# Kernel optimization log

Hardware: AMD Instinct MI355X
Metric: run time of the kernel (lower is better)

The kernel has to match this reference:

```python
import jax, jax.numpy as jnp
import numpy as np

K = 3
KK = K * K
PAD = 1          # kernel_size // 2
MAX_SHIFT = 8.0  # bias_range > 0
DEG = 2          # degrees = (2, 2), paon_type 'a'


def setup_inputs() -> dict:
    key = jax.random.key(0)
    ks = jax.random.split(key, 6)
    B, C, O, H, W = 4, 64, 64, 160, 160
    x = jax.random.normal(ks[0], (B, C, H, W), jnp.float32)
    # offset conv is 1x1: weight [2*K*K, C], bias [2*K*K]
    off_w = jax.random.normal(ks[1], (2 * KK, C), jnp.float32) * 0.1
    off_b = jax.random.normal(ks[2], (2 * KK,), jnp.float32) * 0.1
    scale = 1.0 / np.sqrt(C * KK).astype(np.float32)
    w_m = jax.random.normal(ks[3], (DEG * O, C, K, K), jnp.float32) * scale
    w_n = jax.random.normal(ks[4], (DEG * O, C, K, K), jnp.float32) * scale
    w0 = jax.random.normal(ks[5], (O,), jnp.float32) * 0.1
    return {"x": x, "off_w": off_w, "off_b": off_b, "w_m": w_m, "w_n": w_n, "w0": w0}


def _bilinear_sample(x, py, px):
    """x: [B,C,H,W]; py,px: [B,KK,H,W] -> [B,C,KK,H,W]; zero outside bounds."""
    B, C, H, W = x.shape
    xf = x.reshape(B, C, H * W)
    y0 = jnp.floor(py)
    x0 = jnp.floor(px)
    wy = py - y0
    wx = px - x0
    y0i = y0.astype(jnp.int32)
    x0i = x0.astype(jnp.int32)
    out = jnp.zeros((B, C) + py.shape[1:], x.dtype)
    corners = ((0, 0, (1 - wy) * (1 - wx)), (0, 1, (1 - wy) * wx),
               (1, 0, wy * (1 - wx)), (1, 1, wy * wx))
    for dy, dx, wgt in corners:
        yy = y0i + dy
        xx = x0i + dx
        valid = (yy >= 0) & (yy < H) & (xx >= 0) & (xx < W)
        idx = jnp.clip(yy, 0, H - 1) * W + jnp.clip(xx, 0, W - 1)
        g = jax.vmap(lambda f, i: f[:, i])(xf, idx.reshape(B, -1))  # [B,C,KK*H*W]
        out = out + g.reshape(B, C, *py.shape[1:]) * (wgt * valid)[:, None]
    return out


def _after_poly_a(y, ch, o, take_abs):
    # channel reorder + groupwise sum, per PaLaBase.after_poly_a
    order = np.array([(k * ch) % (ch * o) + k // o for k in range(ch * o)])
    y = y[:, order].reshape(y.shape[0], ch, o, *y.shape[2:])
    return jnp.abs(y).sum(2) if take_abs else y.sum(2)


def reference(x, off_w, off_b, w_m, w_n, w0):
    B, C, H, W = x.shape
    O = w0.shape[0]
    # --- DeformOffset: 1x1 conv -> clamp to image -> tanh soft-limit ---
    off_r = jnp.einsum('bchw,oc->bohw', x, off_w) + off_b[None, :, None, None]
    gy = jnp.arange(H, dtype=x.dtype)[None, None, :, None]
    gx = jnp.arange(W, dtype=x.dtype)[None, None, None, :]
    oy = jnp.clip(off_r[:, 0::2], -gy, H - gy)  # [B,KK,H,W] (dy per kernel pos)
    ox = jnp.clip(off_r[:, 1::2], -gx, W - gx)  # [B,KK,H,W] (dx per kernel pos)
    soft = lambda o: jnp.where(jnp.abs(o) >= MAX_SHIFT,
                               MAX_SHIFT * jnp.tanh(o / MAX_SHIFT), o)
    oy, ox = soft(oy), soft(ox)
    # --- deformable sampling grid (stride=1, dilation=1, zero padding) ---
    kidx = jnp.arange(KK)
    kh = (kidx // K).astype(x.dtype)[None, :, None, None]
    kw = (kidx % K).astype(x.dtype)[None, :, None, None]
    base_y = (jnp.arange(H, dtype=x.dtype) - PAD)[None, None, :, None]
    base_x = (jnp.arange(W, dtype=x.dtype) - PAD)[None, None, None, :]
    py = base_y + kh + oy
    px = base_x + kw + ox
    samp = _bilinear_sample(x, py, px)  # [B,C,KK,H,W]
    # --- Pade numerator / denominator convs on the sampled tensor ---
    pm_raw = jnp.einsum('bckhw,ock->bohw', samp, w_m.reshape(DEG * O, C, KK))
    qn_raw = jnp.einsum('bckhw,ock->bohw', samp, w_n.reshape(DEG * O, C, KK))
    pm = _after_poly_a(pm_raw, O, DEG, take_abs=False)
    qn = _after_poly_a(qn_raw, O, DEG, take_abs=True)
    # prepare_for_div_a: (pm + w0, 1 + qn)
    return (pm + w0[None, :, None, None]) / (1.0 + qn)
```

## Files before the change

### kernel.cpp

```cpp
#include <hip/hip_runtime.h>
#include <hip/hip_bf16.h>
#include <hip/hip_fp16.h>

#define Hh 160
#define Ww 160
#define Cc 64
#define HWc 25600
#define Bb 4
#define AST 76

typedef __attribute__((ext_vector_type(8))) _Float16 half8;
typedef __attribute__((ext_vector_type(4))) float f32x4;

__device__ __forceinline__ unsigned int f2h2u(float a, float b) {
  __half2 h = __floats2half2_rn(a, b);
  return *(unsigned int*)&h;
}

__global__ __launch_bounds__(256) void k_prep(
    const float* __restrict__ x, const float* __restrict__ wm,
    const float* __restrict__ wn, const float* __restrict__ ow,
    unsigned short* __restrict__ xT, unsigned short* __restrict__ bf) {
  if (blockIdx.x < 400) {
    __shared__ unsigned short s[64][260];
    int wg = blockIdx.x;
    int b = wg / 100;
    int pix0 = (wg % 100) * 256;
    int l = threadIdx.x & 63, wv = threadIdx.x >> 6;
    const float* xb = x + (size_t)b * Cc * HWc + pix0;
#pragma unroll
    for (int i = 0; i < 16; i++) {
      int c = i * 4 + wv;
      float4 v = *(const float4*)&xb[(size_t)c * HWc + l * 4];
      *(uint2*)&s[c][l * 4] = make_uint2(f2h2u(v.x, v.y), f2h2u(v.z, v.w));
    }
    __syncthreads();
    int p = threadIdx.x;
    unsigned int w[32];
#pragma unroll
    for (int j = 0; j < 32; j++) {
      unsigned int a = s[2 * j][p];
      unsigned int bb = s[2 * j + 1][p];
      w[j] = (a & 0xffffu) | (bb << 16);
    }
    unsigned short* dst = xT + ((size_t)(b * HWc + pix0 + p)) * 64;
#pragma unroll
    for (int j = 0; j < 8; j++)
      ((uint4*)dst)[j] = make_uint4(w[4 * j], w[4 * j + 1], w[4 * j + 2], w[4 * j + 3]);
  } else {
    int i = (blockIdx.x - 400) * 256 + threadIdx.x;
    if (i < 9 * 2 * 12 * 64 * 8) {
      int j2 = i & 7;
      int lane = (i >> 3) & 63;
      int ntck = i >> 9;
      int nt = ntck % 12;
      int ck = ntck / 12;
      int kk = ck >> 1;
      int chunk = ck & 1;
      int n = nt * 16 + (lane & 15);
      int c = chunk * 32 + (lane >> 4) * 8 + j2;
      float v;
      if (n < 64)
        v = wm[(n * 64 + c) * 9 + kk] + wm[((n + 64) * 64 + c) * 9 + kk];
      else
        v = wn[((n - 64) * 64 + c) * 9 + kk];
      __half hv = __float2half_rn(v);
      bf[i] = *(unsigned short*)&hv;
    } else if (i < 9 * 2 * 12 * 64 * 8 + 2 * 2 * 64 * 8) {
      int j = i - 9 * 2 * 12 * 64 * 8;
      int j2 = j & 7;
      int lane = (j >> 3) & 63;
      int rest = j >> 9;
      int ntile = rest & 1;
      int chunk = rest >> 1;
      int n = ntile * 16 + (lane & 15);
      int c = chunk * 32 + (lane >> 4) * 8 + j2;
      if (n < 18) {
        __half hv = __float2half_rn(ow[n * 64 + c]);
        bf[i] = *(unsigned short*)&hv;
      } else {
        bf[i] = 0;
      }
    }
  }
}

__device__ __forceinline__ void gather_issue(const char* __restrict__ gbase,
                                             uint4 D, int chB, uint4& c00,
                                             uint4& c01, uint4& c10,
                                             uint4& c11) {
  int bb = (int)D.x + chB;
  int dxB = (int)(D.y & 0xffffu);
  int dyB = (int)(D.y >> 16);
  c00 = *(const uint4*)(gbase + bb);
  c01 = *(const uint4*)(gbase + bb + dxB);
  c10 = *(const uint4*)(gbase + bb + dyB);
  c11 = *(const uint4*)(gbase + bb + dxB + dyB);
}

__device__ __forceinline__ void combine_write(unsigned short* Arow, uint2 Wzw,
                                              const uint4& c00, const uint4& c01,
                                              const uint4& c10,
                                              const uint4& c11) {
  __half2 wz = *(const __half2*)&Wzw.x;
  __half2 ww = *(const __half2*)&Wzw.y;
  __half2 W00 = __half2half2(__low2half(wz));
  __half2 W01 = __half2half2(__high2half(wz));
  __half2 W10 = __half2half2(__low2half(ww));
  __half2 W11 = __half2half2(__high2half(ww));
  const unsigned int* a = (const unsigned int*)&c00;
  const unsigned int* b = (const unsigned int*)&c01;
  const unsigned int* c = (const unsigned int*)&c10;
  const unsigned int* d = (const unsigned int*)&c11;
  unsigned int o[4];
#pragma unroll
  for (int j = 0; j < 4; j++) {
    __half2 ha = *(const __half2*)&a[j];
    __half2 hb = *(const __half2*)&b[j];
    __half2 hc = *(const __half2*)&c[j];
    __half2 hd = *(const __half2*)&d[j];
    __half2 r = __hfma2(ha, W00,
                        __hfma2(hb, W01, __hfma2(hc, W10, __hmul2(hd, W11))));
    o[j] = *(unsigned int*)&r;
  }
  *(uint4*)Arow = make_uint4(o[0], o[1], o[2], o[3]);
}

__global__ __launch_bounds__(256, 4) void k_main(
    const unsigned short* __restrict__ xT, const float* __restrict__ w0,
    const float* __restrict__ off_b, const unsigned short* __restrict__ bfrag,
    const unsigned short* __restrict__ obfrag, float* __restrict__ out) {
  __shared__ unsigned short A[3][64 * AST];
  __shared__ uint4 gdesc[576];
  float2* spy = (float2*)&A[0][0];
  const uint2* gdw = (const uint2*)gdesc;
  const int tid = threadIdx.x;
  const int wg = blockIdx.x;
  const int band = wg & 7;
  const int local = wg >> 3;
  const int b = local / 50;
  const int pix0 = band * 3200 + (local % 50) * 64;
  const int wv = tid >> 6;
  const int l = tid & 63;
  const int lm = l & 15;
  const int quad = l >> 4;
  const int ch8 = l & 7;
  const int pr = l >> 3;
  const int chB = ch8 * 16;
  const int pl0 = wv * 16 + pr;
  const int pl1 = wv * 16 + 8 + pr;

  const unsigned short* xTb = xT + (size_t)b * HWc * 64;
  const char* gbase = (const char*)xTb;

  f32x4 acc[3][4];
  const f32x4 zero = {0.f, 0.f, 0.f, 0.f};
#pragma unroll
  for (int j = 0; j < 3; j++)
#pragma unroll
    for (int pt = 0; pt < 4; pt++) acc[j][pt] = zero;

  {
    f32x4 aO0 = zero, aO1 = zero;
    const unsigned short* xrow = xTb + (size_t)(pix0 + wv * 16 + lm) * 64;
#pragma unroll
    for (int chunk = 0; chunk < 2; chunk++) {
      half8 sb = *(const half8*)(xrow + chunk * 32 + quad * 8);
      half8 wf0 = *(const half8*)&obfrag[((chunk * 2 + 0) * 64 + l) * 8];
      half8 wf1 = *(const half8*)&obfrag[((chunk * 2 + 1) * 64 + l) * 8];
      aO0 = __builtin_amdgcn_mfma_f32_16x16x32_f16(wf0, sb, aO0, 0, 0, 0);
      aO1 = __builtin_amdgcn_mfma_f32_16x16x32_f16(wf1, sb, aO1, 0, 0, 0);
    }
    int pix = pix0 + wv * 16 + lm;
    int h = pix / Ww, w = pix % Ww;
    float fh = (float)h, fw = (float)w;
#pragma unroll
    for (int rr = 0; rr < 2; rr++) {
      int n = quad * 4 + 2 * rr;
      int kk = n >> 1;
      float oy = aO0[2 * rr] + off_b[n];
      float ox = aO0[2 * rr + 1] + off_b[n + 1];
      oy = fminf(fmaxf(oy, -fh), 160.0f - fh);
      ox = fminf(fmaxf(ox, -fw), 160.0f - fw);
      if (fabsf(oy) >= 8.0f) oy = 8.0f * tanhf(oy * 0.125f);
      if (fabsf(ox) >= 8.0f) ox = 8.0f * tanhf(ox * 0.125f);
      spy[kk * 64 + wv * 16 + lm] =
          make_float2(fh - 1.0f + (float)(kk / 3) + oy,
                      fw - 1.0f + (float)(kk % 3) + ox);
    }
    if (quad == 0) {
      float oy = aO1[0] + off_b[16];
      float ox = aO1[1] + off_b[17];
      oy = fminf(fmaxf(oy, -fh), 160.0f - fh);
      ox = fminf(fmaxf(ox, -fw), 160.0f - fw);
      if (fabsf(oy) >= 8.0f) oy = 8.0f * tanhf(oy * 0.125f);
      if (fabsf(ox) >= 8.0f) ox = 8.0f * tanhf(ox * 0.125f);
      spy[8 * 64 + wv * 16 + lm] =
          make_float2(fh + 1.0f + oy, fw + 1.0f + ox);
    }
  }
  __syncthreads();

  for (int e = tid; e < 576; e += 256) {
    float2 P = spy[e];
    float py = P.x, pxv = P.y;
    float y0f = floorf(py), x0f = floorf(pxv);
    float wy = py - y0f, wx = pxv - x0f;
    int y0 = (int)y0f, x0 = (int)x0f;
    float vy0 = (y0 >= 0 && y0 < Hh) ? 1.f : 0.f;
    float vy1 = (y0 >= -1 && y0 < Hh - 1) ? 1.f : 0.f;
    float vx0 = (x0 >= 0 && x0 < Ww) ? 1.f : 0.f;
    float vx1 = (x0 >= -1 && x0 < Ww - 1) ? 1.f : 0.f;
    int r0 = min(max(y0, 0), Hh - 1);
    int r1 = min(max(y0 + 1, 0), Hh - 1);
    int c0 = min(max(x0, 0), Ww - 1);
    int c1 = min(max(x0 + 1, 0), Ww - 1);
    float w00 = (1.f - wy) * (1.f - wx) * vy0 * vx0;
    float w01 = (1.f - wy) * wx * vy0 * vx1;
    float w10 = wy * (1.f - wx) * vy1 * vx0;
    float w11 = wy * wx * vy1 * vx1;
    uint4 D;
    D.x = (unsigned int)((r0 * Ww + c0) * 128);
    D.y = (unsigned int)((c1 - c0) * 128) |
          ((unsigned int)((r1 - r0) * Ww * 128) << 16);
    D.z = f2h2u(w00, w01);
    D.w = f2h2u(w10, w11);
    gdesc[e] = D;
  }
  __syncthreads();

  uint4 gA[8], gB[8];
  {
    uint4 D0 = gdesc[pl0], D1 = gdesc[pl1];
    gather_issue(gbase, D0, chB, gA[0], gA[1], gA[2], gA[3]);
    gather_issue(gbase, D1, chB, gA[4], gA[5], gA[6], gA[7]);
    uint4 E0 = gdesc[64 + pl0], E1 = gdesc[64 + pl1];
    gather_issue(gbase, E0, chB, gB[0], gB[1], gB[2], gB[3]);
    gather_issue(gbase, E1, chB, gB[4], gB[5], gB[6], gB[7]);
    combine_write(&A[0][pl0 * AST + ch8 * 8], make_uint2(D0.z, D0.w), gA[0],
                  gA[1], gA[2], gA[3]);
    combine_write(&A[0][pl1 * AST + ch8 * 8], make_uint2(D1.z, D1.w), gA[4],
                  gA[5], gA[6], gA[7]);
  }
  asm volatile("s_waitcnt lgkmcnt(0)" ::: "memory");
  __builtin_amdgcn_s_barrier();

#pragma unroll
  for (int kk = 0; kk < 9; kk++) {
    if (kk < 7) {
      uint4 D0 = gdesc[(kk + 2) * 64 + pl0];
      uint4 D1 = gdesc[(kk + 2) * 64 + pl1];
      if ((kk & 1) == 0) {
        gather_issue(gbase, D0, chB, gA[0], gA[1], gA[2], gA[3]);
        gather_issue(gbase, D1, chB, gA[4], gA[5], gA[6], gA[7]);
      } else {
        gather_issue(gbase, D0, chB, gB[0], gB[1], gB[2], gB[3]);
        gather_issue(gbase, D1, chB, gB[4], gB[5], gB[6], gB[7]);
      }
    }
#pragma unroll
    for (int chunk = 0; chunk < 2; chunk++) {
      half8 sfr[4];
#pragma unroll
      for (int pt = 0; pt < 4; pt++)
        sfr[pt] = *(const half8*)&A[kk % 3][(pt * 16 + lm) * AST + chunk * 32 +
                                            quad * 8];
      half8 wfr[3];
#pragma unroll
      for (int j = 0; j < 3; j++) {
        int nt = j * 4 + wv;
        wfr[j] = *(const half8*)&bfrag[((size_t)((kk * 2 + chunk) * 12 + nt) *
                                           64 + l) * 8];
      }
#pragma unroll
      for (int j = 0; j < 3; j++)
#pragma unroll
        for (int pt = 0; pt < 4; pt++)
          acc[j][pt] = __builtin_amdgcn_mfma_f32_16x16x32_f16(
              wfr[j], sfr[pt], acc[j][pt], 0, 0, 0);
    }
    if (kk < 8) {
      uint2 W0 = gdw[((kk + 1) * 64 + pl0) * 2 + 1];
      uint2 W1 = gdw[((kk + 1) * 64 + pl1) * 2 + 1];
      if (((kk + 1) & 1) == 0) {
        combine_write(&A[(kk + 1) % 3][pl0 * AST + ch8 * 8], W0, gA[0], gA[1],
                      gA[2], gA[3]);
        combine_write(&A[(kk + 1) % 3][pl1 * AST + ch8 * 8], W1, gA[4], gA[5],
                      gA[6], gA[7]);
      } else {
        combine_write(&A[(kk + 1) % 3][pl0 * AST + ch8 * 8], W0, gB[0], gB[1],
                      gB[2], gB[3]);
        combine_write(&A[(kk + 1) % 3][pl1 * AST + ch8 * 8], W1, gB[4], gB[5],
                      gB[6], gB[7]);
      }
      asm volatile("s_waitcnt lgkmcnt(0)" ::: "memory");
      __builtin_amdgcn_s_barrier();
    }
  }

  float w0v[4];
#pragma unroll
  for (int r = 0; r < 4; r++) w0v[r] = w0[wv * 16 + quad * 4 + r];
  float* ob = out + (size_t)b * Cc * HWc + pix0;
#pragma unroll
  for (int pt = 0; pt < 4; pt++) {
#pragma unroll
    for (int r = 0; r < 4; r++) {
      int oc = wv * 16 + quad * 4 + r;
      float pm = acc[0][pt][r] + w0v[r];
      float qn = 1.0f + fabsf(acc[1][pt][r]) + fabsf(acc[2][pt][r]);
      ob[oc * HWc + pt * 16 + lm] = pm / qn;
    }
  }
}

extern "C" void kernel_launch(void* const* d_in, const int* in_sizes, int n_in,
                              void* d_out, int out_size, void* d_ws, size_t ws_size,
                              hipStream_t stream) {
  const float* x = (const float*)d_in[0];
  const float* off_w = (const float*)d_in[1];
  const float* off_b = (const float*)d_in[2];
  const float* w_m = (const float*)d_in[3];
  const float* w_n = (const float*)d_in[4];
  const float* w0 = (const float*)d_in[5];
  float* out = (float*)d_out;

  unsigned short* bfrag = (unsigned short*)d_ws;
  unsigned short* obfrag = (unsigned short*)((char*)d_ws + (size_t)221184);
  unsigned short* xT = (unsigned short*)((char*)d_ws + (size_t)225280);

  hipLaunchKernelGGL(k_prep, dim3(840), dim3(256), 0, stream, x, w_m, w_n,
                     off_w, xT, bfrag);
  hipLaunchKernelGGL(k_main, dim3(1600), dim3(256), 0, stream, xT, w0, off_b,
                     bfrag, obfrag, out);
}
```

Measured before the change: 143.3 us.

## Shrink gather pipeline to double-buffered LDS with single register set

```diff
diff --git a/kernel.cpp b/kernel.cpp
--- a/kernel.cpp
+++ b/kernel.cpp
@@ -130,7 +130,7 @@
     const unsigned short* __restrict__ xT, const float* __restrict__ w0,
     const float* __restrict__ off_b, const unsigned short* __restrict__ bfrag,
     const unsigned short* __restrict__ obfrag, float* __restrict__ out) {
-  __shared__ unsigned short A[3][64 * AST];
+  __shared__ unsigned short A[2][64 * AST];
   __shared__ uint4 gdesc[576];
   float2* spy = (float2*)&A[0][0];
   const uint2* gdw = (const uint2*)gdesc;
@@ -229,42 +229,32 @@
   }
   __syncthreads();
 
-  uint4 gA[8], gB[8];
+  uint4 g[8];
   {
     uint4 D0 = gdesc[pl0], D1 = gdesc[pl1];
-    gather_issue(gbase, D0, chB, gA[0], gA[1], gA[2], gA[3]);
-    gather_issue(gbase, D1, chB, gA[4], gA[5], gA[6], gA[7]);
+    gather_issue(gbase, D0, chB, g[0], g[1], g[2], g[3]);
+    gather_issue(gbase, D1, chB, g[4], g[5], g[6], g[7]);
+    combine_write(&A[0][pl0 * AST + ch8 * 8], make_uint2(D0.z, D0.w), g[0],
+                  g[1], g[2], g[3]);
+    combine_write(&A[0][pl1 * AST + ch8 * 8], make_uint2(D1.z, D1.w), g[4],
+                  g[5], g[6], g[7]);
     uint4 E0 = gdesc[64 + pl0], E1 = gdesc[64 + pl1];
-    gather_issue(gbase, E0, chB, gB[0], gB[1], gB[2], gB[3]);
-    gather_issue(gbase, E1, chB, gB[4], gB[5], gB[6], gB[7]);
-    combine_write(&A[0][pl0 * AST + ch8 * 8], make_uint2(D0.z, D0.w), gA[0],
-                  gA[1], gA[2], gA[3]);
-    combine_write(&A[0][pl1 * AST + ch8 * 8], make_uint2(D1.z, D1.w), gA[4],
-                  gA[5], gA[6], gA[7]);
+    gather_issue(gbase, E0, chB, g[0], g[1], g[2], g[3]);
+    gather_issue(gbase, E1, chB, g[4], g[5], g[6], g[7]);
   }
   asm volatile("s_waitcnt lgkmcnt(0)" ::: "memory");
   __builtin_amdgcn_s_barrier();
 
 #pragma unroll
   for (int kk = 0; kk < 9; kk++) {
-    if (kk < 7) {
-      uint4 D0 = gdesc[(kk + 2) * 64 + pl0];
-      uint4 D1 = gdesc[(kk + 2) * 64 + pl1];
-      if ((kk & 1) == 0) {
-        gather_issue(gbase, D0, chB, gA[0], gA[1], gA[2], gA[3]);
-        gather_issue(gbase, D1, chB, gA[4], gA[5], gA[6], gA[7]);
-      } else {
-        gather_issue(gbase, D0, chB, gB[0], gB[1], gB[2], gB[3]);
-        gather_issue(gbase, D1, chB, gB[4], gB[5], gB[6], gB[7]);
-      }
-    }
+    const int cur = kk & 1;
 #pragma unroll
     for (int chunk = 0; chunk < 2; chunk++) {
       half8 sfr[4];
 #pragma unroll
       for (int pt = 0; pt < 4; pt++)
-        sfr[pt] = *(const half8*)&A[kk % 3][(pt * 16 + lm) * AST + chunk * 32 +
-                                            quad * 8];
+        sfr[pt] = *(const half8*)&A[cur][(pt * 16 + lm) * AST + chunk * 32 +
+                                         quad * 8];
       half8 wfr[3];
 #pragma unroll
       for (int j = 0; j < 3; j++) {
@@ -282,17 +272,18 @@
     if (kk < 8) {
       uint2 W0 = gdw[((kk + 1) * 64 + pl0) * 2 + 1];
       uint2 W1 = gdw[((kk + 1) * 64 + pl1) * 2 + 1];
-      if (((kk + 1) & 1) == 0) {
-        combine_write(&A[(kk + 1) % 3][pl0 * AST + ch8 * 8], W0, gA[0], gA[1],
-                      gA[2], gA[3]);
-        combine_write(&A[(kk + 1) % 3][pl1 * AST + ch8 * 8], W1, gA[4], gA[5],
-                      gA[6], gA[7]);
-      } else {
-        combine_write(&A[(kk + 1) % 3][pl0 * AST + ch8 * 8], W0, gB[0], gB[1],
-                      gB[2], gB[3]);
-        combine_write(&A[(kk + 1) % 3][pl1 * AST + ch8 * 8], W1, gB[4], gB[5],
-                      gB[6], gB[7]);
-      }
+      combine_write(&A[cur ^ 1][pl0 * AST + ch8 * 8], W0, g[0], g[1], g[2],
+                    g[3]);
+      combine_write(&A[cur ^ 1][pl1 * AST + ch8 * 8], W1, g[4], g[5], g[6],
+                    g[7]);
+    }
+    if (kk < 7) {
+      uint4 D0 = gdesc[(kk + 2) * 64 + pl0];
+      uint4 D1 = gdesc[(kk + 2) * 64 + pl1];
+      gather_issue(gbase, D0, chB, g[0], g[1], g[2], g[3]);
+      gather_issue(gbase, D1, chB, g[4], g[5], g[6], g[7]);
+    }
+    if (kk < 8) {
       asm volatile("s_waitcnt lgkmcnt(0)" ::: "memory");
       __builtin_amdgcn_s_barrier();
     }
```

Result: no change. 141.0 us (-1.6%).

## Restructure gather/MFMA pipeline with double-buffered LDS and prefetched weight fragments

Applied to the files above, without the earlier changes.

```diff
diff --git a/kernel.cpp b/kernel.cpp
--- a/kernel.cpp
+++ b/kernel.cpp
@@ -126,11 +126,11 @@
   *(uint4*)Arow = make_uint4(o[0], o[1], o[2], o[3]);
 }
 
-__global__ __launch_bounds__(256, 4) void k_main(
+__global__ __launch_bounds__(256, 2) void k_main(
     const unsigned short* __restrict__ xT, const float* __restrict__ w0,
     const float* __restrict__ off_b, const unsigned short* __restrict__ bfrag,
     const unsigned short* __restrict__ obfrag, float* __restrict__ out) {
-  __shared__ unsigned short A[3][64 * AST];
+  __shared__ unsigned short A[2][64 * AST];
   __shared__ uint4 gdesc[576];
   float2* spy = (float2*)&A[0][0];
   const uint2* gdw = (const uint2*)gdesc;
@@ -230,69 +230,102 @@
   __syncthreads();
 
   uint4 gA[8], gB[8];
+  half8 wfA[2][3], wfB[2][3];
+
+#pragma unroll
+  for (int ch = 0; ch < 2; ch++)
+#pragma unroll
+    for (int j = 0; j < 3; j++) {
+      int nt = j * 4 + wv;
+      wfA[ch][j] =
+          *(const half8*)&bfrag[((size_t)(ch * 12 + nt) * 64 + l) * 8];
+    }
   {
     uint4 D0 = gdesc[pl0], D1 = gdesc[pl1];
     gather_issue(gbase, D0, chB, gA[0], gA[1], gA[2], gA[3]);
     gather_issue(gbase, D1, chB, gA[4], gA[5], gA[6], gA[7]);
-    uint4 E0 = gdesc[64 + pl0], E1 = gdesc[64 + pl1];
-    gather_issue(gbase, E0, chB, gB[0], gB[1], gB[2], gB[3]);
-    gather_issue(gbase, E1, chB, gB[4], gB[5], gB[6], gB[7]);
     combine_write(&A[0][pl0 * AST + ch8 * 8], make_uint2(D0.z, D0.w), gA[0],
                   gA[1], gA[2], gA[3]);
     combine_write(&A[0][pl1 * AST + ch8 * 8], make_uint2(D1.z, D1.w), gA[4],
                   gA[5], gA[6], gA[7]);
-  }
+    uint4 E0 = gdesc[64 + pl0], E1 = gdesc[64 + pl1];
+    gather_issue(gbase, E0, chB, gB[0], gB[1], gB[2], gB[3]);
+    gather_issue(gbase, E1, chB, gB[4], gB[5], gB[6], gB[7]);
+  }
+#pragma unroll
+  for (int ch = 0; ch < 2; ch++)
+#pragma unroll
+    for (int j = 0; j < 3; j++) {
+      int nt = j * 4 + wv;
+      wfB[ch][j] =
+          *(const half8*)&bfrag[((size_t)((2 + ch) * 12 + nt) * 64 + l) * 8];
+    }
   asm volatile("s_waitcnt lgkmcnt(0)" ::: "memory");
   __builtin_amdgcn_s_barrier();
 
 #pragma unroll
   for (int kk = 0; kk < 9; kk++) {
+    const int cur = kk & 1;
+#pragma unroll
+    for (int chunk = 0; chunk < 2; chunk++) {
+      half8 sfr[4];
+#pragma unroll
+      for (int pt = 0; pt < 4; pt++)
+        sfr[pt] = *(const half8*)&A[cur][(pt * 16 + lm) * AST + chunk * 32 +
+                                         quad * 8];
+      if (cur == 0) {
+#pragma unroll
+        for (int j = 0; j < 3; j++)
+#pragma unroll
+          for (int pt = 0; pt < 4; pt++)
+            acc[j][pt] = __builtin_amdgcn_mfma_f32_16x16x32_f16(
+                wfA[chunk][j], sfr[pt], acc[j][pt], 0, 0, 0);
+      } else {
+#pragma unroll
+        for (int j = 0; j < 3; j++)
+#pragma unroll
+          for (int pt = 0; pt < 4; pt++)
+            acc[j][pt] = __builtin_amdgcn_mfma_f32_16x16x32_f16(
+                wfB[chunk][j], sfr[pt], acc[j][pt], 0, 0, 0);
+      }
+    }
+    if (kk < 8) {
+      uint2 W0 = gdw[((kk + 1) * 64 + pl0) * 2 + 1];
+      uint2 W1 = gdw[((kk + 1) * 64 + pl1) * 2 + 1];
+      unsigned short* d0 = &A[cur ^ 1][pl0 * AST + ch8 * 8];
+      unsigned short* d1 = &A[cur ^ 1][pl1 * AST + ch8 * 8];
+      if (cur == 0) {
+        combine_write(d0, W0, gB[0], gB[1], gB[2], gB[3]);
+        combine_write(d1, W1, gB[4], gB[5], gB[6], gB[7]);
+      } else {
+        combine_write(d0, W0, gA[0], gA[1], gA[2], gA[3]);
+        combine_write(d1, W1, gA[4], gA[5], gA[6], gA[7]);
+      }
+    }
     if (kk < 7) {
       uint4 D0 = gdesc[(kk + 2) * 64 + pl0];
       uint4 D1 = gdesc[(kk + 2) * 64 + pl1];
-      if ((kk & 1) == 0) {
+      if (cur == 0) {
         gather_issue(gbase, D0, chB, gA[0], gA[1], gA[2], gA[3]);
         gather_issue(gbase, D1, chB, gA[4], gA[5], gA[6], gA[7]);
       } else {
         gather_issue(gbase, D0, chB, gB[0], gB[1], gB[2], gB[3]);
         gather_issue(gbase, D1, chB, gB[4], gB[5], gB[6], gB[7]);
       }
-    }
-#pragma unroll
-    for (int chunk = 0; chunk < 2; chunk++) {
-      half8 sfr[4];
-#pragma unroll
-      for (int pt = 0; pt < 4; pt++)
-        sfr[pt] = *(const half8*)&A[kk % 3][(pt * 16 + lm) * AST + chunk * 32 +
-                                            quad * 8];
-      half8 wfr[3];
-#pragma unroll
-      for (int j = 0; j < 3; j++) {
-        int nt = j * 4 + wv;
-        wfr[j] = *(const half8*)&bfrag[((size_t)((kk * 2 + chunk) * 12 + nt) *
-                                           64 + l) * 8];
-      }
-#pragma unroll
-      for (int j = 0; j < 3; j++)
-#pragma unroll
-        for (int pt = 0; pt < 4; pt++)
-          acc[j][pt] = __builtin_amdgcn_mfma_f32_16x16x32_f16(
-              wfr[j], sfr[pt], acc[j][pt], 0, 0, 0);
+#pragma unroll
+      for (int ch = 0; ch < 2; ch++)
+#pragma unroll
+        for (int j = 0; j < 3; j++) {
+          int nt = j * 4 + wv;
+          half8 v = *(const half8*)&bfrag[((size_t)(((kk + 2) * 2 + ch) * 12 +
+                                                    nt) * 64 + l) * 8];
+          if (cur == 0)
+            wfA[ch][j] = v;
+          else
+            wfB[ch][j] = v;
+        }
     }
     if (kk < 8) {
-      uint2 W0 = gdw[((kk + 1) * 64 + pl0) * 2 + 1];
-      uint2 W1 = gdw[((kk + 1) * 64 + pl1) * 2 + 1];
-      if (((kk + 1) & 1) == 0) {
-        combine_write(&A[(kk + 1) % 3][pl0 * AST + ch8 * 8], W0, gA[0], gA[1],
-                      gA[2], gA[3]);
-        combine_write(&A[(kk + 1) % 3][pl1 * AST + ch8 * 8], W1, gA[4], gA[5],
-                      gA[6], gA[7]);
-      } else {
-        combine_write(&A[(kk + 1) % 3][pl0 * AST + ch8 * 8], W0, gB[0], gB[1],
-                      gB[2], gB[3]);
-        combine_write(&A[(kk + 1) % 3][pl1 * AST + ch8 * 8], W1, gB[4], gB[5],
-                      gB[6], gB[7]);
-      }
       asm volatile("s_waitcnt lgkmcnt(0)" ::: "memory");
       __builtin_amdgcn_s_barrier();
     }
```

Measured after the change: 131.3 us. 1.09x faster.
